# Performance work log

Hardware: AMD Instinct MI355X
Metric: run time of the kernel (lower is better)

## Reference

```python
import jax, jax.numpy as jnp
import numpy as np
from jax import lax


def setup_inputs() -> dict:
    key = jax.random.key(0)
    B = 8388608  # batch of 2-d states
    N = 200      # number of recurrence steps
    theta = np.pi / 100.0
    # linM = [[cos, sin], [-sin, cos]]; forward uses linM.T
    linM = jnp.array([[np.cos(theta), np.sin(theta)],
                      [-np.sin(theta), np.cos(theta)]], dtype=jnp.float32)
    x = jax.random.normal(key, (B, 2), dtype=jnp.float32)
    return {"x": x, "linMt": linM.T, "N": N}


def reference(x, linMt, N):
    # Faithful to: for _ in range(N): x = x @ linMt
    # Expressed as a single scan (one fused recurrence instead of N launches).
    def step(c, _):
        return jnp.matmul(c, linMt), None
    out, _ = lax.scan(step, x, None, length=N)
    return out
```

## Files before the change

### kernel.cpp

```cpp
#include <hip/hip_runtime.h>


__global__ __launch_bounds__(256)
void lin2d_apply(const float* __restrict__ x,
                 const float* __restrict__ linMt,
                 const int* __restrict__ Nptr,
                 float* __restrict__ out,
                 long long n4, long long ntail_pairs)
{
    float b00 = linMt[0], b01 = linMt[1];
    float b10 = linMt[2], b11 = linMt[3];
    unsigned e = (unsigned)Nptr[0];

    float r00 = 1.f, r01 = 0.f, r10 = 0.f, r11 = 1.f;
    while (e) {
        if (e & 1u) {
            float t00 = r00*b00 + r01*b10;
            float t01 = r00*b01 + r01*b11;
            float t10 = r10*b00 + r11*b10;
            float t11 = r10*b01 + r11*b11;
            r00 = t00; r01 = t01; r10 = t10; r11 = t11;
        }
        e >>= 1;
        if (e) {
            float t00 = b00*b00 + b01*b10;
            float t01 = b00*b01 + b01*b11;
            float t10 = b10*b00 + b11*b10;
            float t11 = b10*b01 + b11*b11;
            b00 = t00; b01 = t01; b10 = t10; b11 = t11;
        }
    }

    const float4* __restrict__ xin = (const float4*)x;
    float4* __restrict__ o = (float4*)out;
    long long idx    = (long long)blockIdx.x * blockDim.x + threadIdx.x;
    long long stride = (long long)gridDim.x * blockDim.x;
    for (long long i = idx; i < n4; i += stride) {
        float4 v = xin[i];
        float4 w;
        w.x = v.x * r00 + v.y * r10;
        w.y = v.x * r01 + v.y * r11;
        w.z = v.z * r00 + v.w * r10;
        w.w = v.z * r01 + v.w * r11;
        o[i] = w;
    }

    if (idx == 0) {
        for (long long p = 0; p < ntail_pairs; ++p) {
            long long base = n4 * 4 + p * 2;
            float x0 = x[base], x1 = x[base + 1];
            out[base]     = x0 * r00 + x1 * r10;
            out[base + 1] = x0 * r01 + x1 * r11;
        }
    }
}

extern "C" void kernel_launch(void* const* d_in, const int* in_sizes, int n_in,
                              void* d_out, int out_size, void* d_ws, size_t ws_size,
                              hipStream_t stream) {
    const float* x     = (const float*)d_in[0];
    const float* linMt = (const float*)d_in[1];
    const int*   N     = (const int*)d_in[2];
    float* out = (float*)d_out;

    long long total = (long long)in_sizes[0];
    long long n4 = total / 4;
    long long ntail_pairs = (total - n4 * 4) / 2;

    lin2d_apply<<<4096, 256, 0, stream>>>(x, linMt, N, out, n4, ntail_pairs);
}
```

Before: 114.5 us.

## Issue nontemporal loads before matrix power and use one-shot two-element-per-thread grid

Replaces the grid-stride loop with a fixed grid where each thread handles two float4 elements. Both loads are issued before the matrix-power computation, so memory latency overlaps the scalar exponentiation. Loads and stores use nontemporal builtins to avoid cache pollution on a pure streaming pass. The trade-off is more blocks, each repeating the small power computation.

```diff
diff --git a/kernel.cpp b/kernel.cpp
--- a/kernel.cpp
+++ b/kernel.cpp
@@ -1,5 +1,7 @@
 #include <hip/hip_runtime.h>
 
+
+typedef float f4 __attribute__((ext_vector_type(4)));
 
 __global__ __launch_bounds__(256)
 void lin2d_apply(const float* __restrict__ x,
@@ -8,10 +10,20 @@
                  float* __restrict__ out,
                  long long n4, long long ntail_pairs)
 {
+    const f4* __restrict__ xin = (const f4*)x;
+    f4* __restrict__ o = (f4*)out;
+
+    long long i0 = (long long)blockIdx.x * 512 + threadIdx.x;
+    long long i1 = i0 + 256;
+    bool h0 = i0 < n4, h1 = i1 < n4;
+
+    f4 v0 = {0.f, 0.f, 0.f, 0.f}, v1 = {0.f, 0.f, 0.f, 0.f};
+    if (h0) v0 = __builtin_nontemporal_load(&xin[i0]);
+    if (h1) v1 = __builtin_nontemporal_load(&xin[i1]);
+
     float b00 = linMt[0], b01 = linMt[1];
     float b10 = linMt[2], b11 = linMt[3];
     unsigned e = (unsigned)Nptr[0];
-
     float r00 = 1.f, r01 = 0.f, r10 = 0.f, r11 = 1.f;
     while (e) {
         if (e & 1u) {
@@ -31,21 +43,24 @@
         }
     }
 
-    const float4* __restrict__ xin = (const float4*)x;
-    float4* __restrict__ o = (float4*)out;
-    long long idx    = (long long)blockIdx.x * blockDim.x + threadIdx.x;
-    long long stride = (long long)gridDim.x * blockDim.x;
-    for (long long i = idx; i < n4; i += stride) {
-        float4 v = xin[i];
-        float4 w;
-        w.x = v.x * r00 + v.y * r10;
-        w.y = v.x * r01 + v.y * r11;
-        w.z = v.z * r00 + v.w * r10;
-        w.w = v.z * r01 + v.w * r11;
-        o[i] = w;
+    if (h0) {
+        f4 w;
+        w.x = v0.x * r00 + v0.y * r10;
+        w.y = v0.x * r01 + v0.y * r11;
+        w.z = v0.z * r00 + v0.w * r10;
+        w.w = v0.z * r01 + v0.w * r11;
+        __builtin_nontemporal_store(w, &o[i0]);
+    }
+    if (h1) {
+        f4 w;
+        w.x = v1.x * r00 + v1.y * r10;
+        w.y = v1.x * r01 + v1.y * r11;
+        w.z = v1.z * r00 + v1.w * r10;
+        w.w = v1.z * r01 + v1.w * r11;
+        __builtin_nontemporal_store(w, &o[i1]);
     }
 
-    if (idx == 0) {
+    if (blockIdx.x == 0 && threadIdx.x == 0) {
         for (long long p = 0; p < ntail_pairs; ++p) {
             long long base = n4 * 4 + p * 2;
             float x0 = x[base], x1 = x[base + 1];
@@ -67,5 +82,7 @@
     long long n4 = total / 4;
     long long ntail_pairs = (total - n4 * 4) / 2;
 
-    lin2d_apply<<<4096, 256, 0, stream>>>(x, linMt, N, out, n4, ntail_pairs);
+    int blocks = (int)((n4 + 511) / 512);
+    if (blocks < 1) blocks = 1;
+    lin2d_apply<<<blocks, 256, 0, stream>>>(x, linMt, N, out, n4, ntail_pairs);
 }
```

Result: slower. 119.7 us (+4.5%).
